# Kernel optimization log

Measured on AMD Instinct MI355X. Metric: run time of the kernel, lower is better.

Reference implementation:

```python
import jax, jax.numpy as jnp
import numpy as np

N_NODES = 100000
N_EDGES = 1600000
IN_CH = 128
OUT_CH = 64
NEG_SLOPE = 0.2
EPS = 1e-10


def setup_inputs() -> dict:
    key = jax.random.key(0)
    k1, k2, k3, k4, k5 = jax.random.split(key, 5)
    x = jax.random.normal(k1, (N_NODES, IN_CH), dtype=jnp.float32)
    edge_index = jax.random.randint(k2, (2, N_EDGES), 0, N_NODES, dtype=jnp.int64)
    W = jax.random.normal(k3, (OUT_CH, IN_CH), dtype=jnp.float32) * (1.0 / np.sqrt(IN_CH))
    a_l = jax.random.normal(k4, (OUT_CH,), dtype=jnp.float32) * (1.0 / np.sqrt(OUT_CH))
    a_r = jax.random.normal(k5, (OUT_CH,), dtype=jnp.float32) * (1.0 / np.sqrt(OUT_CH))
    bias = jnp.zeros((OUT_CH,), dtype=jnp.float32)
    return {"x": x, "edge_index": edge_index, "W": W, "a_l": a_l, "a_r": a_r, "bias": bias}


def reference(x, edge_index, W, a_l, a_r, bias):
    N = x.shape[0]
    h = x @ W.T                     # (N, out_ch)
    src, dst = edge_index[0], edge_index[1]
    e_l = h @ a_l                   # (N,)
    e_r = h @ a_r                   # (N,)
    edge_attn = jax.nn.leaky_relu(e_l[dst] + e_r[src], negative_slope=NEG_SLOPE)  # (E,)
    # segment softmax over incoming edges of each dst node
    edge_max = jax.ops.segment_max(edge_attn, dst, num_segments=N)  # (N,), -inf for isolated
    edge_attn = jnp.exp(edge_attn - edge_max[dst])
    edge_sum = jax.ops.segment_sum(edge_attn, dst, num_segments=N)  # (N,)
    edge_attn = edge_attn / (edge_sum[dst] + EPS)
    messages = h[src] * edge_attn[:, None]                          # (E, out_ch)
    out = jax.ops.segment_sum(messages, dst, num_segments=N)        # (N, out_ch)
    return out + bias
```

## Files before the change

### kernel.cpp

```cpp
#include <hip/hip_runtime.h>
#include <math.h>

#define NN 100000
#define NE 1600000
#define IC 128
#define OC 64
#define NEG_SLOPE 0.2f
#define EPS_F 1e-10f

#define NSLICE 200
#define SN 500
#define EB 500
#define QPB 800
#define CAP 12000

typedef short bf16x8 __attribute__((ext_vector_type(8)));
typedef float f32x4 __attribute__((ext_vector_type(4)));

__device__ __forceinline__ unsigned short f2bf(float f) {
    unsigned u = __float_as_uint(f);
    u += 0x7fff + ((u >> 16) & 1);
    return (unsigned short)(u >> 16);
}

__global__ __launch_bounds__(256) void linear_kernel(
    const float* __restrict__ x, const float* __restrict__ W,
    const float* __restrict__ a_l, const float* __restrict__ a_r,
    unsigned short* __restrict__ h_bf, float* __restrict__ e_l,
    float* __restrict__ e_r)
{
    __shared__ unsigned short lds[128 * 136];
    const int tid = threadIdx.x;
    const int n0 = blockIdx.x * 64;

#pragma unroll
    for (int it = 0; it < 8; it++) {
        int i = it * 256 + tid;
        int r = i >> 5, c4 = i & 31;
        int n = n0 + r;
        float4 v = make_float4(0.f, 0.f, 0.f, 0.f);
        if (n < NN) v = *(const float4*)&x[(size_t)n * 128 + (c4 << 2)];
        ushort4 b;
        b.x = f2bf(v.x); b.y = f2bf(v.y); b.z = f2bf(v.z); b.w = f2bf(v.w);
        *(ushort4*)&lds[r * 136 + (c4 << 2)] = b;
    }
#pragma unroll
    for (int it = 0; it < 8; it++) {
        int i = it * 256 + tid;
        int r = i >> 5, c4 = i & 31;
        float4 v = *(const float4*)&W[r * 128 + (c4 << 2)];
        ushort4 b;
        b.x = f2bf(v.x); b.y = f2bf(v.y); b.z = f2bf(v.z); b.w = f2bf(v.w);
        *(ushort4*)&lds[(64 + r) * 136 + (c4 << 2)] = b;
    }
    __syncthreads();

    const int wv = tid >> 6;
    const int lane = tid & 63;
    const int q = lane >> 4;
    const int c = lane & 15;

    f32x4 acc[4];
#pragma unroll
    for (int t = 0; t < 4; t++) acc[t] = (f32x4){0.f, 0.f, 0.f, 0.f};

    const unsigned short* xrow = &lds[(wv * 16 + c) * 136];
    const unsigned short* wrow = &lds[(64 + c) * 136];

#pragma unroll
    for (int kk = 0; kk < 4; kk++) {
        int ko = kk * 32 + q * 8;
        bf16x8 a = *(const bf16x8*)&xrow[ko];
#pragma unroll
        for (int t = 0; t < 4; t++) {
            bf16x8 b = *(const bf16x8*)&wrow[t * 16 * 136 + ko];
            acc[t] = __builtin_amdgcn_mfma_f32_16x16x32_bf16(a, b, acc[t], 0, 0, 0);
        }
    }

#pragma unroll
    for (int r = 0; r < 4; r++) {
        int m = n0 + wv * 16 + q * 4 + r;
        if (m < NN) {
#pragma unroll
            for (int t = 0; t < 4; t++)
                h_bf[(size_t)m * OC + t * 16 + c] = f2bf(acc[t][r]);
        }
    }

    float al[4], ar[4];
#pragma unroll
    for (int t = 0; t < 4; t++) { al[t] = a_l[t * 16 + c]; ar[t] = a_r[t * 16 + c]; }
    float pl[4], pr[4];
#pragma unroll
    for (int r = 0; r < 4; r++) {
        pl[r] = al[0] * acc[0][r] + al[1] * acc[1][r] + al[2] * acc[2][r] + al[3] * acc[3][r];
        pr[r] = ar[0] * acc[0][r] + ar[1] * acc[1][r] + ar[2] * acc[2][r] + ar[3] * acc[3][r];
    }
#pragma unroll
    for (int m = 1; m < 16; m <<= 1) {
#pragma unroll
        for (int r = 0; r < 4; r++) {
            pl[r] += __shfl_xor(pl[r], m);
            pr[r] += __shfl_xor(pr[r], m);
        }
    }
    if (c == 0) {
#pragma unroll
        for (int r = 0; r < 4; r++) {
            int m = n0 + wv * 16 + q * 4 + r;
            if (m < NN) { e_l[m] = pl[r]; e_r[m] = pr[r]; }
        }
    }
}

__global__ __launch_bounds__(256) void hist_kernel(
    const int* __restrict__ dst, int* __restrict__ H)
{
    __shared__ int hist[NSLICE];
    const int t = threadIdx.x, b = blockIdx.x;
    if (t < NSLICE) hist[t] = 0;
    __syncthreads();
    for (int qi = t; qi < QPB; qi += 256) {
        int4 d = ((const int4*)dst)[b * QPB + qi];
        atomicAdd(&hist[d.x / SN], 1);
        atomicAdd(&hist[d.y / SN], 1);
        atomicAdd(&hist[d.z / SN], 1);
        atomicAdd(&hist[d.w / SN], 1);
    }
    __syncthreads();
    if (t < NSLICE) H[t * EB + b] = hist[t];
}

__global__ __launch_bounds__(1024) void scan_block_kernel(
    const int* __restrict__ deg, int* __restrict__ offsets,
    int* __restrict__ bsums)
{
    __shared__ int wsum[16];
    const int t = threadIdx.x;
    const int lane = t & 63, wv = t >> 6;
    const int i = blockIdx.x * 1024 + t;
    int v = (i < NN) ? deg[i] : 0;
    int incl = v;
#pragma unroll
    for (int off = 1; off < 64; off <<= 1) {
        int u = __shfl_up(incl, off);
        if (lane >= off) incl += u;
    }
    if (lane == 63) wsum[wv] = incl;
    __syncthreads();
    if (wv == 0 && lane < 16) {
        int s = wsum[lane];
        int si = s;
#pragma unroll
        for (int off = 1; off < 16; off <<= 1) {
            int u = __shfl_up(si, off);
            if (lane >= off) si += u;
        }
        wsum[lane] = si - s;
    }
    __syncthreads();
    int excl = incl - v + wsum[wv];
    if (i < NN) offsets[i] = excl;
    if (t == 1023) bsums[blockIdx.x] = excl + v;
}

__global__ __launch_bounds__(128) void scan_bsums_kernel(int* __restrict__ bsums)
{
    __shared__ int s[128];
    const int t = threadIdx.x;
    const int NB = (NN + 1023) / 1024;
    int v = (t < NB) ? bsums[t] : 0;
    s[t] = v;
    __syncthreads();
    for (int off = 1; off < 128; off <<= 1) {
        int u = (t >= off) ? s[t - off] : 0;
        __syncthreads();
        s[t] += u;
        __syncthreads();
    }
    if (t < NB) bsums[t] = s[t] - v;
}

__global__ __launch_bounds__(256) void bucket_kernel(
    const int* __restrict__ src, const int* __restrict__ dst,
    const int* __restrict__ O_raw, const int* __restrict__ bsums,
    int* __restrict__ bucketed)
{
    __shared__ int cur[NSLICE];
    const int t = threadIdx.x, b = blockIdx.x;
    if (t < NSLICE) {
        int gi = t * EB + b;
        cur[t] = O_raw[gi] + bsums[gi >> 10];
    }
    __syncthreads();
    for (int qi = t; qi < QPB; qi += 256) {
        int4 d4 = ((const int4*)dst)[b * QPB + qi];
        int4 s4 = ((const int4*)src)[b * QPB + qi];
        int dd[4] = {d4.x, d4.y, d4.z, d4.w};
        int ss[4] = {s4.x, s4.y, s4.z, s4.w};
#pragma unroll
        for (int k = 0; k < 4; k++) {
            int sl = dd[k] / SN;
            int pos = atomicAdd(&cur[sl], 1);
            bucketed[pos] = ((dd[k] - sl * SN) << 17) | ss[k];
        }
    }
}

__global__ __launch_bounds__(1024) void fine_sort_kernel(
    const int* __restrict__ bucketed, const int* __restrict__ O_raw,
    const int* __restrict__ bsums, const float* __restrict__ e_l,
    const float* __restrict__ e_r, float2* __restrict__ sorted_sw,
    int* __restrict__ offsets_out)
{
    __shared__ int ebuf[CAP];
    __shared__ float wbuf[CAP];
    __shared__ int hist[SN];
    __shared__ float nsum[SN];
    __shared__ float el[SN];
    __shared__ int wsums[8];
    const int s = blockIdx.x, t = threadIdx.x;
    int gi0 = s * EB;
    const int B0 = O_raw[gi0] + bsums[gi0 >> 10];
    int B1 = NE;
    if (s < NSLICE - 1) {
        int gi1 = (s + 1) * EB;
        B1 = O_raw[gi1] + bsums[gi1 >> 10];
    }
    int cnt = B1 - B0;
    if (cnt > CAP) cnt = CAP;

    for (int i = t; i < cnt; i += 1024) ebuf[i] = bucketed[B0 + i];
    if (t < SN) {
        hist[t] = 0;
        nsum[t] = 0.f;
        el[t] = e_l[s * SN + t];
    }
    __syncthreads();
    for (int i = t; i < cnt; i += 1024) {
        int p = ebuf[i];
        int dloc = p >> 17;
        int sr = p & 0x1FFFF;
        float a = el[dloc] + e_r[sr];
        a = (a > 0.f) ? a : NEG_SLOPE * a;
        float w = __expf(a);
        wbuf[i] = w;
        atomicAdd(&hist[dloc], 1);
        atomicAdd(&nsum[dloc], w);
    }
    __syncthreads();

    const int lane = t & 63, w8 = t >> 6;
    int v = (t < SN) ? hist[t] : 0;
    int incl = v;
#pragma unroll
    for (int o = 1; o < 64; o <<= 1) {
        int u = __shfl_up(incl, o);
        if (lane >= o) incl += u;
    }
    if (w8 < 8 && lane == 63) wsums[w8] = incl;
    __syncthreads();
    if (t == 0) {
        int run = 0;
#pragma unroll
        for (int k = 0; k < 8; k++) { int x = wsums[k]; wsums[k] = run; run += x; }
    }
    __syncthreads();
    int excl = incl - v + ((w8 < 8) ? wsums[w8] : 0);

    if (t < SN) offsets_out[s * SN + t] = B0 + excl;
    __syncthreads();
    if (t < SN) hist[t] = excl;
    __syncthreads();
    for (int i = t; i < cnt; i += 1024) {
        int p = ebuf[i];
        int dloc = p >> 17;
        int pos = atomicAdd(&hist[dloc], 1);
        float wn = wbuf[i] / (nsum[dloc] + EPS_F);
        sorted_sw[B0 + pos] = make_float2(__int_as_float(p & 0x1FFFF), wn);
    }
    if (s == 0 && t == 0) offsets_out[NN] = NE;
}

__global__ __launch_bounds__(256) void aggregate_kernel(
    const unsigned short* __restrict__ h_bf, const int* __restrict__ offsets,
    const float2* __restrict__ sorted_sw, const float* __restrict__ bias,
    float* __restrict__ out)
{
    const int node = blockIdx.x * 4 + (threadIdx.x >> 6);
    const int lane = threadIdx.x & 63;
    if (node >= NN) return;
    const int start = offsets[node];
    const int end = offsets[node + 1];
    const int grp = lane >> 3;
    const int ch = (lane & 7) * 8;

    float acc[8] = {0.f, 0.f, 0.f, 0.f, 0.f, 0.f, 0.f, 0.f};

#pragma unroll 2
    for (int j = start; j < end; j += 8) {
        int eidx = j + grp;
        int ej = (eidx < end) ? eidx : end - 1;
        float2 p = sorted_sw[ej];
        float w = (eidx < end) ? p.y : 0.f;
        int s = __float_as_int(p.x);
        uint4 qv = *(const uint4*)&h_bf[(size_t)s * OC + ch];
        acc[0] += w * __uint_as_float(qv.x << 16);
        acc[1] += w * __uint_as_float(qv.x & 0xffff0000u);
        acc[2] += w * __uint_as_float(qv.y << 16);
        acc[3] += w * __uint_as_float(qv.y & 0xffff0000u);
        acc[4] += w * __uint_as_float(qv.z << 16);
        acc[5] += w * __uint_as_float(qv.z & 0xffff0000u);
        acc[6] += w * __uint_as_float(qv.w << 16);
        acc[7] += w * __uint_as_float(qv.w & 0xffff0000u);
    }

#pragma unroll
    for (int m = 8; m <= 32; m <<= 1) {
#pragma unroll
        for (int k = 0; k < 8; k++) acc[k] += __shfl_xor(acc[k], m);
    }

    if (lane < 8) {
        float4 b0 = *(const float4*)&bias[lane * 8];
        float4 b1 = *(const float4*)&bias[lane * 8 + 4];
        float4 o0 = make_float4(acc[0] + b0.x, acc[1] + b0.y,
                                acc[2] + b0.z, acc[3] + b0.w);
        float4 o1 = make_float4(acc[4] + b1.x, acc[5] + b1.y,
                                acc[6] + b1.z, acc[7] + b1.w);
        *(float4*)&out[(size_t)node * OC + lane * 8] = o0;
        *(float4*)&out[(size_t)node * OC + lane * 8 + 4] = o1;
    }
}

extern "C" void kernel_launch(void* const* d_in, const int* in_sizes, int n_in,
                              void* d_out, int out_size, void* d_ws, size_t ws_size,
                              hipStream_t stream)
{
    const float* x = (const float*)d_in[0];
    const int* edge_index = (const int*)d_in[1];
    const float* W = (const float*)d_in[2];
    const float* a_l = (const float*)d_in[3];
    const float* a_r = (const float*)d_in[4];
    const float* bias = (const float*)d_in[5];
    float* out = (float*)d_out;

    const int* src = edge_index;
    const int* dst = edge_index + NE;

    char* w = (char*)d_ws;
    unsigned short* h_bf = (unsigned short*)w;
    size_t off = (size_t)NN * OC * 2;
    float* e_l = (float*)(w + off); off += (size_t)NN * 4;
    float* e_r = (float*)(w + off); off += (size_t)NN * 4;
    int* H = (int*)(w + off);       off += (size_t)NN * 4;
    int* O_raw = (int*)(w + off);   off += (size_t)(NN + 4) * 4;
    int* bsums = (int*)(w + off);   off += 128 * 4;
    int* offsets = (int*)(w + off); off += (size_t)(NN + 4) * 4;
    int* bucketed = (int*)(w + off); off += (size_t)NE * 4;
    float2* sorted_sw = (float2*)(w + off); off += (size_t)NE * 8;

    linear_kernel<<<(NN + 63) / 64, 256, 0, stream>>>(x, W, a_l, a_r, h_bf, e_l, e_r);
    hist_kernel<<<EB, 256, 0, stream>>>(dst, H);
    scan_block_kernel<<<(NN + 1023) / 1024, 1024, 0, stream>>>(H, O_raw, bsums);
    scan_bsums_kernel<<<1, 128, 0, stream>>>(bsums);
    bucket_kernel<<<EB, 256, 0, stream>>>(src, dst, O_raw, bsums, bucketed);
    fine_sort_kernel<<<NSLICE, 1024, 0, stream>>>(bucketed, O_raw, bsums, e_l, e_r,
                                                  sorted_sw, offsets);
    aggregate_kernel<<<(NN + 3) / 4, 256, 0, stream>>>(h_bf, offsets, sorted_sw, bias, out);
}
```

Baseline: 199.1 us.

## Replace global histogram scan with fixed-capacity slice buckets via atomic counters

Merges the histogram and bucketing passes into one kernel. Each block atomically reserves space in per-slice buckets of fixed capacity, which removes the two scan kernels and the extra read of dst. Per-node start and end offsets are now written separately because the slices are no longer contiguous. The aggregate loop is also unrolled by hand to keep two gathers in flight. If a slice receives more edges than CAP, the excess edges are silently dropped, and the bucket order becomes nondeterministic.

```diff
diff --git a/kernel.cpp b/kernel.cpp
--- a/kernel.cpp
+++ b/kernel.cpp
@@ -114,10 +114,12 @@
     }
 }
 
-__global__ __launch_bounds__(256) void hist_kernel(
-    const int* __restrict__ dst, int* __restrict__ H)
+__global__ __launch_bounds__(256) void bucket_kernel(
+    const int* __restrict__ src, const int* __restrict__ dst,
+    int* __restrict__ slice_cnt, int* __restrict__ bucketed)
 {
     __shared__ int hist[NSLICE];
+    __shared__ int cur[NSLICE];
     const int t = threadIdx.x, b = blockIdx.x;
     if (t < NSLICE) hist[t] = 0;
     __syncthreads();
@@ -129,69 +131,10 @@
         atomicAdd(&hist[d.w / SN], 1);
     }
     __syncthreads();
-    if (t < NSLICE) H[t * EB + b] = hist[t];
-}
-
-__global__ __launch_bounds__(1024) void scan_block_kernel(
-    const int* __restrict__ deg, int* __restrict__ offsets,
-    int* __restrict__ bsums)
-{
-    __shared__ int wsum[16];
-    const int t = threadIdx.x;
-    const int lane = t & 63, wv = t >> 6;
-    const int i = blockIdx.x * 1024 + t;
-    int v = (i < NN) ? deg[i] : 0;
-    int incl = v;
-#pragma unroll
-    for (int off = 1; off < 64; off <<= 1) {
-        int u = __shfl_up(incl, off);
-        if (lane >= off) incl += u;
-    }
-    if (lane == 63) wsum[wv] = incl;
-    __syncthreads();
-    if (wv == 0 && lane < 16) {
-        int s = wsum[lane];
-        int si = s;
-#pragma unroll
-        for (int off = 1; off < 16; off <<= 1) {
-            int u = __shfl_up(si, off);
-            if (lane >= off) si += u;
-        }
-        wsum[lane] = si - s;
-    }
-    __syncthreads();
-    int excl = incl - v + wsum[wv];
-    if (i < NN) offsets[i] = excl;
-    if (t == 1023) bsums[blockIdx.x] = excl + v;
-}
-
-__global__ __launch_bounds__(128) void scan_bsums_kernel(int* __restrict__ bsums)
-{
-    __shared__ int s[128];
-    const int t = threadIdx.x;
-    const int NB = (NN + 1023) / 1024;
-    int v = (t < NB) ? bsums[t] : 0;
-    s[t] = v;
-    __syncthreads();
-    for (int off = 1; off < 128; off <<= 1) {
-        int u = (t >= off) ? s[t - off] : 0;
-        __syncthreads();
-        s[t] += u;
-        __syncthreads();
-    }
-    if (t < NB) bsums[t] = s[t] - v;
-}
-
-__global__ __launch_bounds__(256) void bucket_kernel(
-    const int* __restrict__ src, const int* __restrict__ dst,
-    const int* __restrict__ O_raw, const int* __restrict__ bsums,
-    int* __restrict__ bucketed)
-{
-    __shared__ int cur[NSLICE];
-    const int t = threadIdx.x, b = blockIdx.x;
     if (t < NSLICE) {
-        int gi = t * EB + b;
-        cur[t] = O_raw[gi] + bsums[gi >> 10];
+        int h = hist[t];
+        int base = (h > 0) ? atomicAdd(&slice_cnt[t], h) : 0;
+        cur[t] = t * CAP + base;
     }
     __syncthreads();
     for (int qi = t; qi < QPB; qi += 256) {
@@ -203,16 +146,17 @@
         for (int k = 0; k < 4; k++) {
             int sl = dd[k] / SN;
             int pos = atomicAdd(&cur[sl], 1);
-            bucketed[pos] = ((dd[k] - sl * SN) << 17) | ss[k];
+            if (pos < (sl + 1) * CAP)
+                bucketed[pos] = ((dd[k] - sl * SN) << 17) | ss[k];
         }
     }
 }
 
 __global__ __launch_bounds__(1024) void fine_sort_kernel(
-    const int* __restrict__ bucketed, const int* __restrict__ O_raw,
-    const int* __restrict__ bsums, const float* __restrict__ e_l,
-    const float* __restrict__ e_r, float2* __restrict__ sorted_sw,
-    int* __restrict__ offsets_out)
+    const int* __restrict__ bucketed, const int* __restrict__ slice_cnt,
+    const float* __restrict__ e_l, const float* __restrict__ e_r,
+    float2* __restrict__ sorted_sw, int* __restrict__ off_s,
+    int* __restrict__ off_e)
 {
     __shared__ int ebuf[CAP];
     __shared__ float wbuf[CAP];
@@ -221,14 +165,8 @@
     __shared__ float el[SN];
     __shared__ int wsums[8];
     const int s = blockIdx.x, t = threadIdx.x;
-    int gi0 = s * EB;
-    const int B0 = O_raw[gi0] + bsums[gi0 >> 10];
-    int B1 = NE;
-    if (s < NSLICE - 1) {
-        int gi1 = (s + 1) * EB;
-        B1 = O_raw[gi1] + bsums[gi1 >> 10];
-    }
-    int cnt = B1 - B0;
+    const int B0 = s * CAP;
+    int cnt = slice_cnt[s];
     if (cnt > CAP) cnt = CAP;
 
     for (int i = t; i < cnt; i += 1024) ebuf[i] = bucketed[B0 + i];
@@ -269,7 +207,10 @@
     __syncthreads();
     int excl = incl - v + ((w8 < 8) ? wsums[w8] : 0);
 
-    if (t < SN) offsets_out[s * SN + t] = B0 + excl;
+    if (t < SN) {
+        off_s[s * SN + t] = B0 + excl;
+        off_e[s * SN + t] = B0 + excl + v;
+    }
     __syncthreads();
     if (t < SN) hist[t] = excl;
     __syncthreads();
@@ -280,40 +221,51 @@
         float wn = wbuf[i] / (nsum[dloc] + EPS_F);
         sorted_sw[B0 + pos] = make_float2(__int_as_float(p & 0x1FFFF), wn);
     }
-    if (s == 0 && t == 0) offsets_out[NN] = NE;
 }
 
 __global__ __launch_bounds__(256) void aggregate_kernel(
-    const unsigned short* __restrict__ h_bf, const int* __restrict__ offsets,
-    const float2* __restrict__ sorted_sw, const float* __restrict__ bias,
-    float* __restrict__ out)
+    const unsigned short* __restrict__ h_bf, const int* __restrict__ off_s,
+    const int* __restrict__ off_e, const float2* __restrict__ sorted_sw,
+    const float* __restrict__ bias, float* __restrict__ out)
 {
     const int node = blockIdx.x * 4 + (threadIdx.x >> 6);
     const int lane = threadIdx.x & 63;
     if (node >= NN) return;
-    const int start = offsets[node];
-    const int end = offsets[node + 1];
+    const int start = off_s[node];
+    const int end = off_e[node];
     const int grp = lane >> 3;
     const int ch = (lane & 7) * 8;
 
     float acc[8] = {0.f, 0.f, 0.f, 0.f, 0.f, 0.f, 0.f, 0.f};
 
-#pragma unroll 2
-    for (int j = start; j < end; j += 8) {
-        int eidx = j + grp;
-        int ej = (eidx < end) ? eidx : end - 1;
-        float2 p = sorted_sw[ej];
-        float w = (eidx < end) ? p.y : 0.f;
-        int s = __float_as_int(p.x);
-        uint4 qv = *(const uint4*)&h_bf[(size_t)s * OC + ch];
-        acc[0] += w * __uint_as_float(qv.x << 16);
-        acc[1] += w * __uint_as_float(qv.x & 0xffff0000u);
-        acc[2] += w * __uint_as_float(qv.y << 16);
-        acc[3] += w * __uint_as_float(qv.y & 0xffff0000u);
-        acc[4] += w * __uint_as_float(qv.z << 16);
-        acc[5] += w * __uint_as_float(qv.z & 0xffff0000u);
-        acc[6] += w * __uint_as_float(qv.w << 16);
-        acc[7] += w * __uint_as_float(qv.w & 0xffff0000u);
+    for (int j = start; j < end; j += 16) {
+        int e0 = j + grp, e1 = j + 8 + grp;
+        int c0 = (e0 < end) ? e0 : end - 1;
+        int c1 = (e1 < end) ? e1 : end - 1;
+        float2 p0 = sorted_sw[c0];
+        float2 p1 = sorted_sw[c1];
+        int s0 = __float_as_int(p0.x);
+        int s1 = __float_as_int(p1.x);
+        uint4 q0 = *(const uint4*)&h_bf[(size_t)s0 * OC + ch];
+        uint4 q1 = *(const uint4*)&h_bf[(size_t)s1 * OC + ch];
+        float w0 = (e0 < end) ? p0.y : 0.f;
+        float w1 = (e1 < end) ? p1.y : 0.f;
+        acc[0] += w0 * __uint_as_float(q0.x << 16);
+        acc[1] += w0 * __uint_as_float(q0.x & 0xffff0000u);
+        acc[2] += w0 * __uint_as_float(q0.y << 16);
+        acc[3] += w0 * __uint_as_float(q0.y & 0xffff0000u);
+        acc[4] += w0 * __uint_as_float(q0.z << 16);
+        acc[5] += w0 * __uint_as_float(q0.z & 0xffff0000u);
+        acc[6] += w0 * __uint_as_float(q0.w << 16);
+        acc[7] += w0 * __uint_as_float(q0.w & 0xffff0000u);
+        acc[0] += w1 * __uint_as_float(q1.x << 16);
+        acc[1] += w1 * __uint_as_float(q1.x & 0xffff0000u);
+        acc[2] += w1 * __uint_as_float(q1.y << 16);
+        acc[3] += w1 * __uint_as_float(q1.y & 0xffff0000u);
+        acc[4] += w1 * __uint_as_float(q1.z << 16);
+        acc[5] += w1 * __uint_as_float(q1.z & 0xffff0000u);
+        acc[6] += w1 * __uint_as_float(q1.w << 16);
+        acc[7] += w1 * __uint_as_float(q1.w & 0xffff0000u);
     }
 
 #pragma unroll
@@ -352,21 +304,20 @@
     char* w = (char*)d_ws;
     unsigned short* h_bf = (unsigned short*)w;
     size_t off = (size_t)NN * OC * 2;
-    float* e_l = (float*)(w + off); off += (size_t)NN * 4;
-    float* e_r = (float*)(w + off); off += (size_t)NN * 4;
-    int* H = (int*)(w + off);       off += (size_t)NN * 4;
-    int* O_raw = (int*)(w + off);   off += (size_t)(NN + 4) * 4;
-    int* bsums = (int*)(w + off);   off += 128 * 4;
-    int* offsets = (int*)(w + off); off += (size_t)(NN + 4) * 4;
-    int* bucketed = (int*)(w + off); off += (size_t)NE * 4;
-    float2* sorted_sw = (float2*)(w + off); off += (size_t)NE * 8;
+    float* e_l = (float*)(w + off);  off += (size_t)NN * 4;
+    float* e_r = (float*)(w + off);  off += (size_t)NN * 4;
+    int* slice_cnt = (int*)(w + off); off += 256 * 4;
+    int* off_s = (int*)(w + off);    off += (size_t)NN * 4;
+    int* off_e = (int*)(w + off);    off += (size_t)NN * 4;
+    int* bucketed = (int*)(w + off); off += (size_t)NSLICE * CAP * 4;
+    float2* sorted_sw = (float2*)(w + off); off += (size_t)NSLICE * CAP * 8;
+
+    hipMemsetAsync(slice_cnt, 0, 256 * 4, stream);
 
     linear_kernel<<<(NN + 63) / 64, 256, 0, stream>>>(x, W, a_l, a_r, h_bf, e_l, e_r);
-    hist_kernel<<<EB, 256, 0, stream>>>(dst, H);
-    scan_block_kernel<<<(NN + 1023) / 1024, 1024, 0, stream>>>(H, O_raw, bsums);
-    scan_bsums_kernel<<<1, 128, 0, stream>>>(bsums);
-    bucket_kernel<<<EB, 256, 0, stream>>>(src, dst, O_raw, bsums, bucketed);
-    fine_sort_kernel<<<NSLICE, 1024, 0, stream>>>(bucketed, O_raw, bsums, e_l, e_r,
-                                                  sorted_sw, offsets);
-    aggregate_kernel<<<(NN + 3) / 4, 256, 0, stream>>>(h_bf, offsets, sorted_sw, bias, out);
-}
+    bucket_kernel<<<EB, 256, 0, stream>>>(src, dst, slice_cnt, bucketed);
+    fine_sort_kernel<<<NSLICE, 1024, 0, stream>>>(bucketed, slice_cnt, e_l, e_r,
+                                                  sorted_sw, off_s, off_e);
+    aggregate_kernel<<<(NN + 3) / 4, 256, 0, stream>>>(h_bf, off_s, off_e,
+                                                       sorted_sw, bias, out);
+}
```

Result: no change. 201.4 us (+1.2%).
